# Kernel tuning notes

Measured on AMD Instinct MI355X. Metric: run time of the kernel, lower is better.

The kernel has to match this reference:

```python
import jax, jax.numpy as jnp
import numpy as np


def setup_inputs() -> dict:
    key = jax.random.key(0)
    ks = jax.random.split(key, 8)
    B, S, H, I = 2, 1025, 3200, 12800
    T = B * S
    # int8 tensors represented as int32, symmetric range [-128, 126]
    hidden_states = jax.random.randint(ks[0], (B, S, H), 0, 255, dtype=jnp.int32) - 127
    scale_in = (jax.random.uniform(ks[1], (T,)) * 0.02 + 1e-4).astype(jnp.float16)
    w1 = jax.random.randint(ks[2], (I, H), 0, 255, dtype=jnp.int32) - 127
    w1_scale = (jax.random.uniform(ks[3], (I,)) * 0.01 + 1e-4).astype(jnp.float32)
    b1 = (jax.random.normal(ks[4], (I,)) * 0.02).astype(jnp.float16)
    w2 = jax.random.randint(ks[5], (H, I), 0, 255, dtype=jnp.int32) - 127
    w2_scale = (jax.random.uniform(ks[6], (H,)) * 0.01 + 1e-4).astype(jnp.float32)
    b2 = (jax.random.normal(ks[7], (H,)) * 0.02).astype(jnp.float16)
    return {"hidden_states": hidden_states, "scale_in": scale_in,
            "w1": w1, "w1_scale": w1_scale, "b1": b1,
            "w2": w2, "w2_scale": w2_scale, "b2": b2}


def _w8a8_linear(x_int, scale_x, w_int, w_scale, bias):
    # int8 GEMM with int32 accumulation, dequant with per-token * per-channel scales
    acc = jnp.matmul(x_int, w_int.T)  # [T, out] int32
    out = acc.astype(jnp.float32) * scale_x[:, None].astype(jnp.float32) * w_scale[None, :]
    return (out + bias.astype(jnp.float32)).astype(jnp.float16)


def _gelu_and_quant(x_f16):
    # fused GELU + per-token dynamic symmetric int8 quantization
    g = jax.nn.gelu(x_f16.astype(jnp.float32), approximate=False)  # [T, I]
    amax = jnp.max(jnp.abs(g), axis=-1)                              # [T]
    scale_act = (amax / 127.0).astype(jnp.float16)
    s = jnp.maximum(scale_act.astype(jnp.float32), 1e-8)
    q = jnp.clip(jnp.round(g / s[:, None]), -128, 127).astype(jnp.int32)
    return q, scale_act


def reference(hidden_states, scale_in, w1, w1_scale, b1, w2, w2_scale, b2):
    B, S, H = hidden_states.shape
    x = hidden_states.reshape(-1, H)               # [T, H] int
    fc1_out = _w8a8_linear(x, scale_in, w1, w1_scale, b1)      # [T, I] fp16
    act_out, scale_act = _gelu_and_quant(fc1_out)              # int8-as-int32, [T] fp16
    fc2_out = _w8a8_linear(act_out, scale_act, w2, w2_scale, b2)  # [T, H] fp16
    return fc2_out
```

## Files before the change

kernel.cpp:

```cpp
#include <hip/hip_runtime.h>
#include <hip/hip_fp16.h>

typedef int v4i __attribute__((ext_vector_type(4)));

#define AS1C(p) ((const __attribute__((address_space(1))) void*)(p))
#define AS3(p)  ((__attribute__((address_space(3))) void*)(p))
#define BARRIER() do { __builtin_amdgcn_s_barrier(); asm volatile("" ::: "memory"); } while (0)

template <int EPI, int BM>
__launch_bounds__(512, 1)
__global__ void gemm_fat(const signed char* __restrict__ A, const signed char* __restrict__ Bw,
                         int M, int N, int K,
                         const float* __restrict__ scale_tok, const float* __restrict__ wsc,
                         const float* __restrict__ bias,
                         __half* __restrict__ gout, unsigned int* __restrict__ amax,
                         float* __restrict__ fout) {
  constexpr int ACH = BM / 16;
  constexpr int CT  = ACH + 16;
  constexpr int CPW = CT / 8;
  constexpr int TB  = CT * 1024;
  constexpr int MI  = BM / 32;
  constexpr int MH  = MI / 2;
  __shared__ __align__(16) char smem[4 * TB];

  const int tid = threadIdx.x;
  const int lane = tid & 63, wave = tid >> 6;
  const int wavem = wave >> 2, waven = wave & 3;

  const int gy = gridDim.y;
  int lid;
  {
    const int o = blockIdx.y * gridDim.x + blockIdx.x;
    const int nwg = gridDim.x * gy;
    const int q = nwg >> 3, r = nwg & 7;
    const int x = o & 7, p = o >> 3;
    lid = (x < r ? x * (q + 1) : r * (q + 1) + (x - r) * q) + p;
  }
  const long long t0 = (long long)(lid % gy) * BM;
  const long long n0 = (long long)(lid / gy) * 256;
  const int nk = K >> 6;

  const signed char* sp[CPW];
  int dst[CPW];
#pragma unroll
  for (int i = 0; i < CPW; ++i) {
    const int c = wave * CPW + i;
    const bool isA = c < ACH;
    const int lr = (isA ? c : c - ACH) * 16 + (lane >> 2);
    const int gslot = (((lane & 3) ^ ((lr >> 1) & 3)) << 4);
    long long gr = isA ? (t0 + lr) : (n0 + lr);
    const long long rmax = (isA ? (long long)M : (long long)N) - 1;
    if (gr > rmax) gr = rmax;
    sp[i] = (isA ? A : Bw) + gr * (long long)K + gslot;
    dst[i] = c * 1024;
  }

#define STAGE(bi) do { \
    _Pragma("unroll") \
    for (int i = 0; i < CPW; ++i) { \
      __builtin_amdgcn_global_load_lds(AS1C(sp[i]), AS3(&smem[(bi) * TB + dst[i]]), 16, 0, 0); \
      sp[i] += 64; \
    } \
  } while (0)

  const int lh = lane & 15;
  const int xs = (((lane >> 4) ^ ((lh >> 1) & 3)) << 4);
  const int offA = wavem * (BM / 2) * 64 + lh * 64 + xs;
  const int offB = ACH * 1024 + waven * 4096 + lh * 64 + xs;

  v4i acc[MI][4] = {};

  STAGE(0);
  if (nk > 1) STAGE(1);
  if (nk > 2) STAGE(2);

  int cur = 0;
  for (int t = 0; t < nk; ++t) {
    if (t < nk - 2) {
      if constexpr (CPW == 4) asm volatile("s_waitcnt vmcnt(8)" ::: "memory");
      else                    asm volatile("s_waitcnt vmcnt(6)" ::: "memory");
    } else if (t == nk - 2) {
      if constexpr (CPW == 4) asm volatile("s_waitcnt vmcnt(4)" ::: "memory");
      else                    asm volatile("s_waitcnt vmcnt(3)" ::: "memory");
    } else {
      asm volatile("s_waitcnt vmcnt(0)" ::: "memory");
    }
    BARRIER();

    const char* base = &smem[cur * TB];
    if (t + 3 < nk) STAGE((cur + 3) & 3);

    v4i b_[4], a0_[MH], a1_[MH];
#pragma unroll
    for (int mi = 0; mi < MH; ++mi) a0_[mi] = *(const v4i*)(base + offA + mi * 1024);
#pragma unroll
    for (int ni = 0; ni < 4; ++ni) b_[ni] = *(const v4i*)(base + offB + ni * 1024);

    __builtin_amdgcn_s_setprio(1);
#pragma unroll
    for (int mi = 0; mi < MH; ++mi)
#pragma unroll
      for (int ni = 0; ni < 4; ++ni)
        acc[mi][ni] = __builtin_amdgcn_mfma_i32_16x16x64_i8(a0_[mi], b_[ni], acc[mi][ni], 0, 0, 0);
    __builtin_amdgcn_s_setprio(0);

#pragma unroll
    for (int mi = 0; mi < MH; ++mi) a1_[mi] = *(const v4i*)(base + offA + (MH + mi) * 1024);

    __builtin_amdgcn_s_setprio(1);
#pragma unroll
    for (int mi = 0; mi < MH; ++mi)
#pragma unroll
      for (int ni = 0; ni < 4; ++ni)
        acc[MH + mi][ni] = __builtin_amdgcn_mfma_i32_16x16x64_i8(a1_[mi], b_[ni], acc[MH + mi][ni], 0, 0, 0);
    __builtin_amdgcn_s_setprio(0);

    cur = (cur + 1) & 3;
  }
#undef STAGE

  long long cidx[4]; float w4[4], bi4[4]; bool cok[4];
#pragma unroll
  for (int ni = 0; ni < 4; ++ni) {
    cidx[ni] = n0 + waven * 64 + ni * 16 + lh;
    cok[ni] = cidx[ni] < N;
    w4[ni] = cok[ni] ? wsc[cidx[ni]] : 0.f;
    bi4[ni] = cok[ni] ? bias[cidx[ni]] : 0.f;
  }
  if (EPI == 0) {
#pragma unroll
    for (int mi = 0; mi < MI; ++mi) {
#pragma unroll
      for (int j = 0; j < 4; ++j) {
        const long long t = t0 + wavem * (BM / 2) + mi * 16 + (lane >> 4) * 4 + j;
        const bool valid = t < M;
        const float st = valid ? scale_tok[t] : 0.f;
        float rowmax = 0.f;
#pragma unroll
        for (int ni = 0; ni < 4; ++ni) {
          float v = (float)acc[mi][ni][j] * st * w4[ni] + bi4[ni];
          v = __half2float(__float2half(v));
          const float gl = 0.5f * v * (1.f + erff(v * 0.70710678118654752f));
          rowmax = fmaxf(rowmax, fabsf(gl));
          if (valid && cok[ni]) gout[t * (long long)N + cidx[ni]] = __float2half(gl);
        }
#pragma unroll
        for (int m = 1; m < 16; m <<= 1) rowmax = fmaxf(rowmax, __shfl_xor(rowmax, m));
        if (valid && lh == 0) atomicMax(&amax[t], __float_as_uint(rowmax));
      }
    }
  } else {
#pragma unroll
    for (int mi = 0; mi < MI; ++mi) {
#pragma unroll
      for (int j = 0; j < 4; ++j) {
        const long long t = t0 + wavem * (BM / 2) + mi * 16 + (lane >> 4) * 4 + j;
        if (t < M) {
          const float am = __uint_as_float(amax[t]);
          const float st = __half2float(__float2half(am * (1.f / 127.f)));
#pragma unroll
          for (int ni = 0; ni < 4; ++ni) {
            const float v = (float)acc[mi][ni][j] * st * w4[ni] + bi4[ni];
            if (cok[ni]) fout[t * (long long)N + cidx[ni]] = __half2float(__float2half(v));
          }
        }
      }
    }
  }
}

__global__ void pack_all(const int* __restrict__ a, const int* __restrict__ b,
                         const int* __restrict__ c,
                         signed char* __restrict__ pa, signed char* __restrict__ pb,
                         signed char* __restrict__ pc,
                         unsigned int* __restrict__ amax,
                         long long na, long long nb, long long nc, int T) {
  const long long gid = blockIdx.x * (long long)blockDim.x + threadIdx.x;
  if (gid < T) amax[gid] = 0u;
  const long long n4a = na >> 2, n4b = nb >> 2, n4c = nc >> 2;
  const long long tot = n4a + n4b + n4c;
  const long long stride = (long long)gridDim.x * blockDim.x;
  for (long long u = gid; u < tot; u += stride) {
    const int* src; signed char* dst; long long loc;
    if (u < n4a)            { src = a; dst = pa; loc = u; }
    else if (u < n4a + n4b) { src = b; dst = pb; loc = u - n4a; }
    else                    { src = c; dst = pc; loc = u - n4a - n4b; }
    const int4 v = *(const int4*)(src + (loc << 2));
    const unsigned out = (unsigned)(v.x & 0xff) | ((unsigned)(v.y & 0xff) << 8) |
                         ((unsigned)(v.z & 0xff) << 16) | ((unsigned)(v.w & 0xff) << 24);
    *(unsigned*)(dst + (loc << 2)) = out;
  }
}

__global__ void gelu_quant(const __half* __restrict__ g, const unsigned int* __restrict__ amax,
                           signed char* __restrict__ q, long long total, int I) {
  const long long nchunk = total >> 3;
  const long long stride = (long long)gridDim.x * blockDim.x;
  for (long long c = blockIdx.x * (long long)blockDim.x + threadIdx.x; c < nchunk; c += stride) {
    const long long base = c << 3;
    const int t = (int)(base / I);
    const float am = __uint_as_float(amax[t]);
    const float s = fmaxf(__half2float(__float2half(am * (1.f / 127.f))), 1e-8f);
    const float inv = 1.f / s;
    const int4 raw = *(const int4*)(g + base);
    const __half2* h2 = (const __half2*)&raw;
    union { signed char b[8]; int2 v; } u;
#pragma unroll
    for (int k = 0; k < 4; ++k) {
      const float2 f = __half22float2(h2[k]);
      const float q0 = fminf(fmaxf(rintf(f.x * inv), -128.f), 127.f);
      const float q1 = fminf(fmaxf(rintf(f.y * inv), -128.f), 127.f);
      u.b[k * 2]     = (signed char)(int)q0;
      u.b[k * 2 + 1] = (signed char)(int)q1;
    }
    *(int2*)(q + base) = u.v;
  }
}

extern "C" void kernel_launch(void* const* d_in, const int* in_sizes, int n_in,
                              void* d_out, int out_size, void* d_ws, size_t ws_size,
                              hipStream_t stream) {
  const int* hs = (const int*)d_in[0];
  const float* scale_in = (const float*)d_in[1];
  const int* w1 = (const int*)d_in[2];
  const float* w1s = (const float*)d_in[3];
  const float* b1 = (const float*)d_in[4];
  const int* w2 = (const int*)d_in[5];
  const float* w2s = (const float*)d_in[6];
  const float* b2 = (const float*)d_in[7];

  const int T = in_sizes[1];
  const int I = in_sizes[3];
  const int H = in_sizes[6];

  char* ws = (char*)d_ws;
  unsigned int* amax = (unsigned int*)ws;
  signed char* px  = (signed char*)(ws + 16384);
  signed char* pw1 = px + (size_t)T * H;
  signed char* pw2 = pw1 + (size_t)I * H;
  __half* gbuf = (__half*)(pw2 + (size_t)H * I);
  signed char* qbuf = (signed char*)(gbuf + (size_t)T * I);

  const long long nx = (long long)T * H, nw1 = (long long)I * H, nw2 = (long long)H * I;

  pack_all<<<2048, 256, 0, stream>>>(hs, w1, w2, px, pw1, pw2, amax, nx, nw1, nw2, T);

  dim3 g1(I / 256, (T + 255) / 256);
  gemm_fat<0, 256><<<g1, 512, 0, stream>>>(px, pw1, T, I, H, scale_in, w1s, b1, gbuf, amax, nullptr);

  gelu_quant<<<2048, 256, 0, stream>>>(gbuf, amax, qbuf, (long long)T * I, I);

  dim3 g2((H + 255) / 256, (T + 127) / 128);
  gemm_fat<1, 128><<<g2, 512, 0, stream>>>(qbuf, pw2, T, H, I, nullptr, w2s, b2, nullptr, amax, (float*)d_out);
}
```

Before: 374.5 us.

## Load A operand directly into registers and stage only B through LDS

Replaces the GEMM's LDS staging of the activation (A) tile with direct global-to-register loads, double-buffered across an unrolled pair of iterations. Only the weight (B) tile still goes through a 4-slot LDS ring via global_load_lds. The aim is to cut LDS footprint and LDS read traffic for A. The cost is that A is no longer shared in LDS across the four N-waves, so each wave re-reads it from global/L2. Also, the vmcnt(2) fences now sit behind the A register loads, which shortens the effective prefetch depth and exposes more global latency.

```diff
diff --git a/kernel.cpp b/kernel.cpp
--- a/kernel.cpp
+++ b/kernel.cpp
@@ -7,25 +7,27 @@
 #define AS3(p)  ((__attribute__((address_space(3))) void*)(p))
 #define BARRIER() do { __builtin_amdgcn_s_barrier(); asm volatile("" ::: "memory"); } while (0)
 
+__device__ __forceinline__ void fence_vm(int n) {
+  if (n >= 4)      asm volatile("s_waitcnt vmcnt(4)" ::: "memory");
+  else if (n >= 2) asm volatile("s_waitcnt vmcnt(2)" ::: "memory");
+  else             asm volatile("s_waitcnt vmcnt(0)" ::: "memory");
+}
+
 template <int EPI, int BM>
 __launch_bounds__(512, 1)
-__global__ void gemm_fat(const signed char* __restrict__ A, const signed char* __restrict__ Bw,
-                         int M, int N, int K,
-                         const float* __restrict__ scale_tok, const float* __restrict__ wsc,
-                         const float* __restrict__ bias,
-                         __half* __restrict__ gout, unsigned int* __restrict__ amax,
-                         float* __restrict__ fout) {
-  constexpr int ACH = BM / 16;
-  constexpr int CT  = ACH + 16;
-  constexpr int CPW = CT / 8;
-  constexpr int TB  = CT * 1024;
-  constexpr int MI  = BM / 32;
-  constexpr int MH  = MI / 2;
-  __shared__ __align__(16) char smem[4 * TB];
+__global__ void gemm_areg(const signed char* __restrict__ A, const signed char* __restrict__ Bw,
+                          int M, int N, int K,
+                          const float* __restrict__ scale_tok, const float* __restrict__ wsc,
+                          const float* __restrict__ bias,
+                          __half* __restrict__ gout, unsigned int* __restrict__ amax,
+                          float* __restrict__ fout) {
+  constexpr int MI = BM / 32;
+  __shared__ __align__(16) char smem[4 * 16384];
 
   const int tid = threadIdx.x;
   const int lane = tid & 63, wave = tid >> 6;
   const int wavem = wave >> 2, waven = wave & 3;
+  const int lh = lane & 15;
 
   const int gy = gridDim.y;
   int lid;
@@ -40,84 +42,76 @@
   const long long n0 = (long long)(lid / gy) * 256;
   const int nk = K >> 6;
 
-  const signed char* sp[CPW];
-  int dst[CPW];
-#pragma unroll
-  for (int i = 0; i < CPW; ++i) {
-    const int c = wave * CPW + i;
-    const bool isA = c < ACH;
-    const int lr = (isA ? c : c - ACH) * 16 + (lane >> 2);
+  const long long Mm1 = M - 1, Nm1 = N - 1;
+  const signed char* pA[MI];
+#pragma unroll
+  for (int mi = 0; mi < MI; ++mi) {
+    long long r = t0 + wavem * (BM / 2) + mi * 16 + lh;
+    if (r > Mm1) r = Mm1;
+    pA[mi] = A + r * (long long)K + ((lane >> 4) << 4);
+  }
+
+  const signed char* spB[2];
+  int dstB[2];
+#pragma unroll
+  for (int i = 0; i < 2; ++i) {
+    const int c = wave * 2 + i;
+    const int lr = c * 16 + (lane >> 2);
     const int gslot = (((lane & 3) ^ ((lr >> 1) & 3)) << 4);
-    long long gr = isA ? (t0 + lr) : (n0 + lr);
-    const long long rmax = (isA ? (long long)M : (long long)N) - 1;
-    if (gr > rmax) gr = rmax;
-    sp[i] = (isA ? A : Bw) + gr * (long long)K + gslot;
-    dst[i] = c * 1024;
-  }
-
-#define STAGE(bi) do { \
+    long long gr = n0 + lr;
+    if (gr > Nm1) gr = Nm1;
+    spB[i] = Bw + gr * (long long)K + gslot;
+    dstB[i] = c * 1024;
+  }
+
+#define STB(sl) do { \
+    __builtin_amdgcn_global_load_lds(AS1C(spB[0]), AS3(&smem[(sl) * 16384 + dstB[0]]), 16, 0, 0); spB[0] += 64; \
+    __builtin_amdgcn_global_load_lds(AS1C(spB[1]), AS3(&smem[(sl) * 16384 + dstB[1]]), 16, 0, 0); spB[1] += 64; \
+  } while (0)
+
+  const int xs = (((lane >> 4) ^ ((lh >> 1) & 3)) << 4);
+  const int offB = waven * 4096 + lh * 64 + xs;
+
+  v4i acc[MI][4] = {};
+  v4i aA[MI], aB[MI], b_[4];
+
+#pragma unroll
+  for (int mi = 0; mi < MI; ++mi) { aA[mi] = *(const v4i*)pA[mi]; pA[mi] += 64; }
+  STB(0);
+  if (nk > 1) STB(1);
+  if (nk > 2) STB(2);
+
+#define ITER(T, AU, AL) do { \
+    const int T_ = (T); \
+    fence_vm(T_ == 0 ? (nk > 2 ? 4 : (nk > 1 ? 2 : 0)) : ((T_ + 2 < nk) ? 2 : 0)); \
+    BARRIER(); \
+    if (T_ + 1 < nk) { \
+      _Pragma("unroll") \
+      for (int mi = 0; mi < MI; ++mi) { AL[mi] = *(const v4i*)pA[mi]; pA[mi] += 64; } \
+    } \
+    if (T_ + 3 < nk) STB((T_ + 3) & 3); \
+    { \
+      const char* bb = &smem[(T_ & 3) * 16384]; \
+      _Pragma("unroll") \
+      for (int ni = 0; ni < 4; ++ni) b_[ni] = *(const v4i*)(bb + offB + ni * 1024); \
+    } \
+    __builtin_amdgcn_s_setprio(1); \
     _Pragma("unroll") \
-    for (int i = 0; i < CPW; ++i) { \
-      __builtin_amdgcn_global_load_lds(AS1C(sp[i]), AS3(&smem[(bi) * TB + dst[i]]), 16, 0, 0); \
-      sp[i] += 64; \
-    } \
+    for (int mi = 0; mi < MI; ++mi) \
+      _Pragma("unroll") \
+      for (int ni = 0; ni < 4; ++ni) \
+        acc[mi][ni] = __builtin_amdgcn_mfma_i32_16x16x64_i8(AU[mi], b_[ni], acc[mi][ni], 0, 0, 0); \
+    __builtin_amdgcn_s_setprio(0); \
   } while (0)
 
-  const int lh = lane & 15;
-  const int xs = (((lane >> 4) ^ ((lh >> 1) & 3)) << 4);
-  const int offA = wavem * (BM / 2) * 64 + lh * 64 + xs;
-  const int offB = ACH * 1024 + waven * 4096 + lh * 64 + xs;
-
-  v4i acc[MI][4] = {};
-
-  STAGE(0);
-  if (nk > 1) STAGE(1);
-  if (nk > 2) STAGE(2);
-
-  int cur = 0;
-  for (int t = 0; t < nk; ++t) {
-    if (t < nk - 2) {
-      if constexpr (CPW == 4) asm volatile("s_waitcnt vmcnt(8)" ::: "memory");
-      else                    asm volatile("s_waitcnt vmcnt(6)" ::: "memory");
-    } else if (t == nk - 2) {
-      if constexpr (CPW == 4) asm volatile("s_waitcnt vmcnt(4)" ::: "memory");
-      else                    asm volatile("s_waitcnt vmcnt(3)" ::: "memory");
-    } else {
-      asm volatile("s_waitcnt vmcnt(0)" ::: "memory");
-    }
-    BARRIER();
-
-    const char* base = &smem[cur * TB];
-    if (t + 3 < nk) STAGE((cur + 3) & 3);
-
-    v4i b_[4], a0_[MH], a1_[MH];
-#pragma unroll
-    for (int mi = 0; mi < MH; ++mi) a0_[mi] = *(const v4i*)(base + offA + mi * 1024);
-#pragma unroll
-    for (int ni = 0; ni < 4; ++ni) b_[ni] = *(const v4i*)(base + offB + ni * 1024);
-
-    __builtin_amdgcn_s_setprio(1);
-#pragma unroll
-    for (int mi = 0; mi < MH; ++mi)
-#pragma unroll
-      for (int ni = 0; ni < 4; ++ni)
-        acc[mi][ni] = __builtin_amdgcn_mfma_i32_16x16x64_i8(a0_[mi], b_[ni], acc[mi][ni], 0, 0, 0);
-    __builtin_amdgcn_s_setprio(0);
-
-#pragma unroll
-    for (int mi = 0; mi < MH; ++mi) a1_[mi] = *(const v4i*)(base + offA + (MH + mi) * 1024);
-
-    __builtin_amdgcn_s_setprio(1);
-#pragma unroll
-    for (int mi = 0; mi < MH; ++mi)
-#pragma unroll
-      for (int ni = 0; ni < 4; ++ni)
-        acc[MH + mi][ni] = __builtin_amdgcn_mfma_i32_16x16x64_i8(a1_[mi], b_[ni], acc[MH + mi][ni], 0, 0, 0);
-    __builtin_amdgcn_s_setprio(0);
-
-    cur = (cur + 1) & 3;
-  }
-#undef STAGE
+  int t = 0;
+  for (; t + 1 < nk; t += 2) {
+    ITER(t, aA, aB);
+    ITER(t + 1, aB, aA);
+  }
+  if (t < nk) ITER(t, aA, aB);
+#undef ITER
+#undef STB
 
   long long cidx[4]; float w4[4], bi4[4]; bool cok[4];
 #pragma unroll
@@ -132,9 +126,9 @@
     for (int mi = 0; mi < MI; ++mi) {
 #pragma unroll
       for (int j = 0; j < 4; ++j) {
-        const long long t = t0 + wavem * (BM / 2) + mi * 16 + (lane >> 4) * 4 + j;
-        const bool valid = t < M;
-        const float st = valid ? scale_tok[t] : 0.f;
+        const long long t2 = t0 + wavem * (BM / 2) + mi * 16 + (lane >> 4) * 4 + j;
+        const bool valid = t2 < M;
+        const float st = valid ? scale_tok[t2] : 0.f;
         float rowmax = 0.f;
 #pragma unroll
         for (int ni = 0; ni < 4; ++ni) {
@@ -142,11 +136,11 @@
           v = __half2float(__float2half(v));
           const float gl = 0.5f * v * (1.f + erff(v * 0.70710678118654752f));
           rowmax = fmaxf(rowmax, fabsf(gl));
-          if (valid && cok[ni]) gout[t * (long long)N + cidx[ni]] = __float2half(gl);
+          if (valid && cok[ni]) gout[t2 * (long long)N + cidx[ni]] = __float2half(gl);
         }
 #pragma unroll
         for (int m = 1; m < 16; m <<= 1) rowmax = fmaxf(rowmax, __shfl_xor(rowmax, m));
-        if (valid && lh == 0) atomicMax(&amax[t], __float_as_uint(rowmax));
+        if (valid && lh == 0) atomicMax(&amax[t2], __float_as_uint(rowmax));
       }
     }
   } else {
@@ -154,14 +148,14 @@
     for (int mi = 0; mi < MI; ++mi) {
 #pragma unroll
       for (int j = 0; j < 4; ++j) {
-        const long long t = t0 + wavem * (BM / 2) + mi * 16 + (lane >> 4) * 4 + j;
-        if (t < M) {
-          const float am = __uint_as_float(amax[t]);
+        const long long t2 = t0 + wavem * (BM / 2) + mi * 16 + (lane >> 4) * 4 + j;
+        if (t2 < M) {
+          const float am = __uint_as_float(amax[t2]);
           const float st = __half2float(__float2half(am * (1.f / 127.f)));
 #pragma unroll
           for (int ni = 0; ni < 4; ++ni) {
             const float v = (float)acc[mi][ni][j] * st * w4[ni] + bi4[ni];
-            if (cok[ni]) fout[t * (long long)N + cidx[ni]] = __half2float(__float2half(v));
+            if (cok[ni]) fout[t2 * (long long)N + cidx[ni]] = __half2float(__float2half(v));
           }
         }
       }
@@ -246,10 +240,10 @@
   pack_all<<<2048, 256, 0, stream>>>(hs, w1, w2, px, pw1, pw2, amax, nx, nw1, nw2, T);
 
   dim3 g1(I / 256, (T + 255) / 256);
-  gemm_fat<0, 256><<<g1, 512, 0, stream>>>(px, pw1, T, I, H, scale_in, w1s, b1, gbuf, amax, nullptr);
+  gemm_areg<0, 256><<<g1, 512, 0, stream>>>(px, pw1, T, I, H, scale_in, w1s, b1, gbuf, amax, nullptr);
 
   gelu_quant<<<2048, 256, 0, stream>>>(gbuf, amax, qbuf, (long long)T * I, I);
 
   dim3 g2((H + 255) / 256, (T + 127) / 128);
-  gemm_fat<1, 128><<<g2, 512, 0, stream>>>(qbuf, pw2, T, H, I, nullptr, w2s, b2, nullptr, amax, (float*)d_out);
-}
+  gemm_areg<1, 128><<<g2, 512, 0, stream>>>(qbuf, pw2, T, H, I, nullptr, w2s, b2, nullptr, amax, (float*)d_out);
+}
```

New measurement: 670.1 us. 1.79x slower.

## Split global-to-LDS prefetch across MFMA phases with ping-pong barriers

Applied to the files above, without the earlier changes.

Reworks the int8 GEMM main loop so the prefetch of the next stage's global-to-LDS loads is split into halves placed between the two MFMA phases, with barriers bracketing each MFMA block. This follows a ping-pong style schedule that aims to interleave memory issue with matrix-core work across waves. The vmcnt wait now comes at the end of each iteration for the next stage rather than at the start. It adds extra barriers per iteration, which can cost synchronisation overhead.

```diff
diff --git a/kernel.cpp b/kernel.cpp
--- a/kernel.cpp
+++ b/kernel.cpp
@@ -9,23 +9,22 @@
 
 template <int EPI, int BM>
 __launch_bounds__(512, 1)
-__global__ void gemm_fat(const signed char* __restrict__ A, const signed char* __restrict__ Bw,
-                         int M, int N, int K,
-                         const float* __restrict__ scale_tok, const float* __restrict__ wsc,
-                         const float* __restrict__ bias,
-                         __half* __restrict__ gout, unsigned int* __restrict__ amax,
-                         float* __restrict__ fout) {
-  constexpr int ACH = BM / 16;
-  constexpr int CT  = ACH + 16;
-  constexpr int CPW = CT / 8;
-  constexpr int TB  = CT * 1024;
-  constexpr int MI  = BM / 32;
-  constexpr int MH  = MI / 2;
+__global__ void gemm_m201(const signed char* __restrict__ A, const signed char* __restrict__ Bw,
+                          int M, int N, int K,
+                          const float* __restrict__ scale_tok, const float* __restrict__ wsc,
+                          const float* __restrict__ bias,
+                          __half* __restrict__ gout, unsigned int* __restrict__ amax,
+                          float* __restrict__ fout) {
+  constexpr int ABYTES = BM * 64;
+  constexpr int TB = ABYTES + 16384;
+  constexpr int L = TB / (512 * 16);
+  constexpr int MI = BM / 32;
   __shared__ __align__(16) char smem[4 * TB];
 
   const int tid = threadIdx.x;
   const int lane = tid & 63, wave = tid >> 6;
   const int wavem = wave >> 2, waven = wave & 3;
+  const int lh = lane & 15;
 
   const int gy = gridDim.y;
   int lid;
@@ -39,85 +38,112 @@
   const long long t0 = (long long)(lid % gy) * BM;
   const long long n0 = (long long)(lid / gy) * 256;
   const int nk = K >> 6;
-
-  const signed char* sp[CPW];
-  int dst[CPW];
-#pragma unroll
-  for (int i = 0; i < CPW; ++i) {
-    const int c = wave * CPW + i;
-    const bool isA = c < ACH;
-    const int lr = (isA ? c : c - ACH) * 16 + (lane >> 2);
+  const long long Mm1 = M - 1, Nm1 = N - 1;
+
+  const signed char* sp[L];
+  int dst[L];
+#pragma unroll
+  for (int i = 0; i < L; ++i) {
+    const int c = wave * L + i;
+    const bool isA = c < (ABYTES / 1024);
+    const int lr = (isA ? c : c - ABYTES / 1024) * 16 + (lane >> 2);
     const int gslot = (((lane & 3) ^ ((lr >> 1) & 3)) << 4);
     long long gr = isA ? (t0 + lr) : (n0 + lr);
-    const long long rmax = (isA ? (long long)M : (long long)N) - 1;
+    const long long rmax = isA ? Mm1 : Nm1;
     if (gr > rmax) gr = rmax;
     sp[i] = (isA ? A : Bw) + gr * (long long)K + gslot;
     dst[i] = c * 1024;
   }
 
-#define STAGE(bi) do { \
+#define STG(sl, i) do { \
+    __builtin_amdgcn_global_load_lds(AS1C(sp[i]), AS3(&smem[(sl) * TB + dst[i]]), 16, 0, 0); \
+    sp[i] += 64; \
+  } while (0)
+
+  const int xs = (((lane >> 4) ^ ((lh >> 1) & 3)) << 4);
+  const int offA = wavem * (BM / 2) * 64 + lh * 64 + xs;
+  const int offB = ABYTES + waven * 4096 + lh * 64 + xs;
+
+  v4i acc[MI][4] = {};
+  v4i a_[4], b_[4];
+
+#define MFMA16(AOFS) do { \
+    __builtin_amdgcn_s_setprio(1); \
     _Pragma("unroll") \
-    for (int i = 0; i < CPW; ++i) { \
-      __builtin_amdgcn_global_load_lds(AS1C(sp[i]), AS3(&smem[(bi) * TB + dst[i]]), 16, 0, 0); \
-      sp[i] += 64; \
+    for (int mi = 0; mi < 4; ++mi) \
+      _Pragma("unroll") \
+      for (int ni = 0; ni < 4; ++ni) \
+        acc[(AOFS) + mi][ni] = __builtin_amdgcn_mfma_i32_16x16x64_i8(a_[mi], b_[ni], acc[(AOFS) + mi][ni], 0, 0, 0); \
+    __builtin_amdgcn_s_setprio(0); \
+  } while (0)
+
+#define FENCE_NEXT(T_) do { \
+    if ((T_) + 1 < nk) { \
+      if ((T_) + 3 < nk)      { if constexpr (BM == 256) asm volatile("s_waitcnt vmcnt(8)" ::: "memory"); \
+                                else                     asm volatile("s_waitcnt vmcnt(6)" ::: "memory"); } \
+      else if ((T_) + 2 < nk) { if constexpr (BM == 256) asm volatile("s_waitcnt vmcnt(4)" ::: "memory"); \
+                                else                     asm volatile("s_waitcnt vmcnt(3)" ::: "memory"); } \
+      else                    asm volatile("s_waitcnt vmcnt(0)" ::: "memory"); \
     } \
   } while (0)
 
-  const int lh = lane & 15;
-  const int xs = (((lane >> 4) ^ ((lh >> 1) & 3)) << 4);
-  const int offA = wavem * (BM / 2) * 64 + lh * 64 + xs;
-  const int offB = ACH * 1024 + waven * 4096 + lh * 64 + xs;
-
-  v4i acc[MI][4] = {};
-
-  STAGE(0);
-  if (nk > 1) STAGE(1);
-  if (nk > 2) STAGE(2);
-
-  int cur = 0;
+#pragma unroll
+  for (int i = 0; i < L; ++i) STG(0, i);
+#pragma unroll
+  for (int i = 0; i < L; ++i) STG(1, i);
+#pragma unroll
+  for (int i = 0; i < L; ++i) STG(2, i);
+  if constexpr (BM == 256) asm volatile("s_waitcnt vmcnt(8)" ::: "memory");
+  else                     asm volatile("s_waitcnt vmcnt(6)" ::: "memory");
+  BARRIER();
+
   for (int t = 0; t < nk; ++t) {
-    if (t < nk - 2) {
-      if constexpr (CPW == 4) asm volatile("s_waitcnt vmcnt(8)" ::: "memory");
-      else                    asm volatile("s_waitcnt vmcnt(6)" ::: "memory");
-    } else if (t == nk - 2) {
-      if constexpr (CPW == 4) asm volatile("s_waitcnt vmcnt(4)" ::: "memory");
-      else                    asm volatile("s_waitcnt vmcnt(3)" ::: "memory");
+    const int sl = t & 3;
+    const int slw = (t + 3) & 3;
+    const char* base = &smem[sl * TB];
+    const bool pf = (t + 3) < nk;
+
+    if constexpr (BM == 256) {
+      a_[0] = *(const v4i*)(base + offA);
+      a_[1] = *(const v4i*)(base + offA + 1024);
+      a_[2] = *(const v4i*)(base + offA + 2048);
+      a_[3] = *(const v4i*)(base + offA + 3072);
+      b_[0] = *(const v4i*)(base + offB);
+      b_[1] = *(const v4i*)(base + offB + 1024);
+      b_[2] = *(const v4i*)(base + offB + 2048);
+      b_[3] = *(const v4i*)(base + offB + 3072);
+      if (pf) { STG(slw, 0); STG(slw, 1); }
+      BARRIER();
+      MFMA16(0);
+      BARRIER();
+      a_[0] = *(const v4i*)(base + offA + 4096);
+      a_[1] = *(const v4i*)(base + offA + 5120);
+      a_[2] = *(const v4i*)(base + offA + 6144);
+      a_[3] = *(const v4i*)(base + offA + 7168);
+      if (pf) { STG(slw, 2); STG(slw, 3); }
+      FENCE_NEXT(t);
+      BARRIER();
+      MFMA16(4);
+      BARRIER();
     } else {
-      asm volatile("s_waitcnt vmcnt(0)" ::: "memory");
-    }
-    BARRIER();
-
-    const char* base = &smem[cur * TB];
-    if (t + 3 < nk) STAGE((cur + 3) & 3);
-
-    v4i b_[4], a0_[MH], a1_[MH];
-#pragma unroll
-    for (int mi = 0; mi < MH; ++mi) a0_[mi] = *(const v4i*)(base + offA + mi * 1024);
-#pragma unroll
-    for (int ni = 0; ni < 4; ++ni) b_[ni] = *(const v4i*)(base + offB + ni * 1024);
-
-    __builtin_amdgcn_s_setprio(1);
-#pragma unroll
-    for (int mi = 0; mi < MH; ++mi)
-#pragma unroll
-      for (int ni = 0; ni < 4; ++ni)
-        acc[mi][ni] = __builtin_amdgcn_mfma_i32_16x16x64_i8(a0_[mi], b_[ni], acc[mi][ni], 0, 0, 0);
-    __builtin_amdgcn_s_setprio(0);
-
-#pragma unroll
-    for (int mi = 0; mi < MH; ++mi) a1_[mi] = *(const v4i*)(base + offA + (MH + mi) * 1024);
-
-    __builtin_amdgcn_s_setprio(1);
-#pragma unroll
-    for (int mi = 0; mi < MH; ++mi)
-#pragma unroll
-      for (int ni = 0; ni < 4; ++ni)
-        acc[MH + mi][ni] = __builtin_amdgcn_mfma_i32_16x16x64_i8(a1_[mi], b_[ni], acc[MH + mi][ni], 0, 0, 0);
-    __builtin_amdgcn_s_setprio(0);
-
-    cur = (cur + 1) & 3;
-  }
-#undef STAGE
+      a_[0] = *(const v4i*)(base + offA);
+      a_[1] = *(const v4i*)(base + offA + 1024);
+      a_[2] = *(const v4i*)(base + offA + 2048);
+      a_[3] = *(const v4i*)(base + offA + 3072);
+      b_[0] = *(const v4i*)(base + offB);
+      b_[1] = *(const v4i*)(base + offB + 1024);
+      b_[2] = *(const v4i*)(base + offB + 2048);
+      b_[3] = *(const v4i*)(base + offB + 3072);
+      if (pf) { STG(slw, 0); STG(slw, 1); STG(slw, 2); }
+      FENCE_NEXT(t);
+      BARRIER();
+      MFMA16(0);
+      BARRIER();
+    }
+  }
+#undef STG
+#undef MFMA16
+#undef FENCE_NEXT
 
   long long cidx[4]; float w4[4], bi4[4]; bool cok[4];
 #pragma unroll
@@ -246,10 +272,10 @@
   pack_all<<<2048, 256, 0, stream>>>(hs, w1, w2, px, pw1, pw2, amax, nx, nw1, nw2, T);
 
   dim3 g1(I / 256, (T + 255) / 256);
-  gemm_fat<0, 256><<<g1, 512, 0, stream>>>(px, pw1, T, I, H, scale_in, w1s, b1, gbuf, amax, nullptr);
+  gemm_m201<0, 256><<<g1, 512, 0, stream>>>(px, pw1, T, I, H, scale_in, w1s, b1, gbuf, amax, nullptr);
 
   gelu_quant<<<2048, 256, 0, stream>>>(gbuf, amax, qbuf, (long long)T * I, I);
 
   dim3 g2((H + 255) / 256, (T + 127) / 128);
-  gemm_fat<1, 128><<<g2, 512, 0, stream>>>(qbuf, pw2, T, H, I, nullptr, w2s, b2, nullptr, amax, (float*)d_out);
-}
+  gemm_m201<1, 128><<<g2, 512, 0, stream>>>(qbuf, pw2, T, H, I, nullptr, w2s, b2, nullptr, amax, (float*)d_out);
+}
```

Measured after the change: 378.5 us. About the same (+1.1%).
